# Kernel tuning notes

Measured on AMD Instinct MI355X. Metric: run time of the kernel, lower is better.

Reference implementation:

```python
import jax, jax.numpy as jnp
import numpy as np

# Larq ste_sign: forward sign(x) with sign(0)=+1; backward is identity clipped to |x|<=1 (STE).
@jax.custom_vjp
def ste_sign(x):
    return jnp.where(x >= 0, jnp.ones((), x.dtype), -jnp.ones((), x.dtype))

def _ste_fwd(x):
    return ste_sign(x), x

def _ste_bwd(x, g):
    return (g * (jnp.abs(x) <= 1).astype(g.dtype),)

ste_sign.defvjp(_ste_fwd, _ste_bwd)


def setup_inputs() -> dict:
    key = jax.random.key(0)
    k1, k2 = jax.random.split(key)
    x = jax.random.normal(k1, (16, 112, 112, 256), dtype=jnp.float32)      # NHWC
    kernel = jax.random.normal(k2, (3, 3, 256, 1), dtype=jnp.float32) * 0.1  # (kh, kw, C, mult)
    return {"x": x, "kernel": kernel}


def reference(x, kernel):
    # Quantize input and depthwise kernel, then standard depthwise conv (stride 1, SAME, no bias).
    xq = ste_sign(x)
    kq = ste_sign(kernel)
    kh, kw, C, mult = kernel.shape
    rhs = kq.reshape(kh, kw, 1, C * mult)  # HWIO layout for grouped conv
    out = jax.lax.conv_general_dilated(
        xq, rhs,
        window_strides=(1, 1),
        padding="SAME",
        feature_group_count=C,
        dimension_numbers=("NHWC", "HWIO", "NHWC"),
    )
    return out
```

## Files before the change

kernel.cpp:

```cpp
#include <hip/hip_runtime.h>


constexpr int N = 16, H = 112, W = 112, C = 256;
constexpr int TW = 14;
constexpr int COLS = TW + 2;
constexpr int RW = 4;

typedef float f32x4 __attribute__((ext_vector_type(4)));

__global__ __launch_bounds__(256, 4) void bsign_dw3x3_tstore(
        const float* __restrict__ x, const float* __restrict__ k,
        float* __restrict__ out) {
    __shared__ unsigned sig[COLS * C];

    const int lane = threadIdx.x & 63;
    const int wq   = threadIdx.x >> 6;
    const int c0   = lane << 2;
    const int h0   = blockIdx.y * 16;
    const int w0   = blockIdx.x * TW;
    const int n    = blockIdx.z;

    const size_t rowstride = (size_t)W * C;
    const bool ptop = (h0 > 0);
    const bool pbot = (h0 + 16 < H);

    const int ciB = wq << 2;
    const float* xbase = x + (size_t)(n * H + h0 - 1) * rowstride + c0;
    bool cv[4];
    const float* cp[4];
#pragma unroll
    for (int q = 0; q < 4; ++q) {
        const int xc = w0 - 1 + ciB + q;
        cv[q] = (xc >= 0 && xc < W);
        cp[q] = xbase + (ptrdiff_t)xc * (ptrdiff_t)C;
    }
    unsigned sq[4][4] = {{0,0,0,0},{0,0,0,0},{0,0,0,0},{0,0,0,0}};
#pragma unroll
    for (int p = 0; p < 18; ++p) {
        if (p == 0  && !ptop) continue;
        if (p == 17 && !pbot) continue;
        const size_t ro = (size_t)p * rowstride;
#pragma unroll
        for (int q = 0; q < 4; ++q) {
            if (cv[q]) {
                const uint4 v = *reinterpret_cast<const uint4*>(cp[q] + ro);
                sq[q][0] |= (v.x >> 31) << p;
                sq[q][1] |= (v.y >> 31) << p;
                sq[q][2] |= (v.z >> 31) << p;
                sq[q][3] |= (v.w >> 31) << p;
            }
        }
    }
#pragma unroll
    for (int q = 0; q < 4; ++q) {
        uint4 sv; sv.x = sq[q][0]; sv.y = sq[q][1]; sv.z = sq[q][2]; sv.w = sq[q][3];
        *reinterpret_cast<uint4*>(&sig[(ciB + q) * C + c0]) = sv;
    }

    unsigned k3[3][4] = {{0,0,0,0},{0,0,0,0},{0,0,0,0}};
#pragma unroll
    for (int t = 0; t < 9; ++t) {
        const uint4 kv = *reinterpret_cast<const uint4*>(k + t * C + c0);
        const int kr = t / 3, kj = t % 3;
        k3[kj][0] |= (kv.x >> 31) << kr;
        k3[kj][1] |= (kv.y >> 31) << kr;
        k3[kj][2] |= (kv.z >> 31) << kr;
        k3[kj][3] |= (kv.w >> 31) << kr;
    }
    __syncthreads();

    const int hbase = h0 + (wq << 2);
    float* obase = out + (size_t)(n * H + hbase) * rowstride
                       + (size_t)w0 * C + c0;
    const bool ledge = (w0 == 0), redge = (w0 + TW == W);

#pragma unroll
    for (int r = 0; r < RW; ++r) {
        const int h  = hbase + r;
        const unsigned b = (h == 0) ? 6u : (h == H - 1) ? 3u : 7u;
        const int nr = (h == 0 || h == H - 1) ? 2 : 3;
        const int sh = (wq << 2) + r;
        float* orow = obase + (size_t)r * rowstride;

        int t0m2[4], t0m1[4], t1m1[4], tj0[4], tj1[4], tj2[4];

        auto tcol = [&](int ci) {
            const uint4 v = *reinterpret_cast<const uint4*>(&sig[ci * C + c0]);
            const unsigned d[4] = {v.x >> sh, v.y >> sh, v.z >> sh, v.w >> sh};
#pragma unroll
            for (int ch = 0; ch < 4; ++ch) {
                tj0[ch] = nr - 2 * __popc((d[ch] ^ k3[0][ch]) & b);
                tj1[ch] = nr - 2 * __popc((d[ch] ^ k3[1][ch]) & b);
                tj2[ch] = nr - 2 * __popc((d[ch] ^ k3[2][ch]) & b);
            }
        };

        if (ledge) {
#pragma unroll
            for (int ch = 0; ch < 4; ++ch) t0m2[ch] = 0;
        } else {
            tcol(0);
#pragma unroll
            for (int ch = 0; ch < 4; ++ch) t0m2[ch] = tj0[ch];
        }
        tcol(1);
#pragma unroll
        for (int ch = 0; ch < 4; ++ch) { t0m1[ch] = tj0[ch]; t1m1[ch] = tj1[ch]; }

#pragma unroll
        for (int ci = 2; ci < COLS; ++ci) {
            if (ci == COLS - 1 && redge) {
#pragma unroll
                for (int ch = 0; ch < 4; ++ch) tj2[ch] = 0;
            } else {
                tcol(ci);
            }
            f32x4 ov;
#pragma unroll
            for (int ch = 0; ch < 4; ++ch)
                ov[ch] = (float)(t0m2[ch] + t1m1[ch] + tj2[ch]);
            *reinterpret_cast<f32x4*>(orow + (size_t)(ci - 2) * C) = ov;
#pragma unroll
            for (int ch = 0; ch < 4; ++ch) {
                t0m2[ch] = t0m1[ch]; t0m1[ch] = tj0[ch]; t1m1[ch] = tj1[ch];
            }
        }
    }
}

extern "C" void kernel_launch(void* const* d_in, const int* in_sizes, int n_in,
                              void* d_out, int out_size, void* d_ws, size_t ws_size,
                              hipStream_t stream) {
    const float* x = (const float*)d_in[0];
    const float* k = (const float*)d_in[1];
    float* out = (float*)d_out;

    dim3 grid(W / TW, H / 16, N);
    bsign_dw3x3_tstore<<<grid, 256, 0, stream>>>(x, k, out);
}
```

Baseline: 368.6 us.

## Split into sign-packing pass and bit-based conv kernel using workspace

Replaces the fused tiled kernel with two launches. The first packs input signs into 32-bit words in a workspace buffer. The second computes the depthwise conv from the packed bits, one block per row, reading neighbouring rows from global memory. This removes the halo re-reads of full fp32 input and the shared-memory staging. In exchange it adds an extra launch and a workspace round trip, and the conv kernel does scattered 4-byte loads. A direct unfused kernel is kept as a fallback when no workspace is available.

```diff
diff --git a/kernel.cpp b/kernel.cpp
--- a/kernel.cpp
+++ b/kernel.cpp
@@ -2,60 +2,35 @@
 
 
 constexpr int N = 16, H = 112, W = 112, C = 256;
-constexpr int TW = 14;
-constexpr int COLS = TW + 2;
-constexpr int RW = 4;
+constexpr int NWORDS = N * H * W * (C / 32);
 
 typedef float f32x4 __attribute__((ext_vector_type(4)));
 
-__global__ __launch_bounds__(256, 4) void bsign_dw3x3_tstore(
-        const float* __restrict__ x, const float* __restrict__ k,
+__global__ __launch_bounds__(256, 4) void pack_signs(
+        const float* __restrict__ x, unsigned* __restrict__ sw) {
+    const int t = blockIdx.x * 256 + threadIdx.x;
+    const float* p = x + (size_t)t * 32;
+    unsigned wv = 0;
+#pragma unroll
+    for (int i = 0; i < 8; ++i) {
+        const uint4 v = *reinterpret_cast<const uint4*>(p + i * 4);
+        wv |= ((v.x >> 31) << (4 * i))     | ((v.y >> 31) << (4 * i + 1))
+            | ((v.z >> 31) << (4 * i + 2)) | ((v.w >> 31) << (4 * i + 3));
+    }
+    sw[t] = wv;
+}
+
+__global__ __launch_bounds__(256, 4) void conv_from_bits(
+        const unsigned* __restrict__ sw, const float* __restrict__ k,
         float* __restrict__ out) {
-    __shared__ unsigned sig[COLS * C];
-
+    const int h    = blockIdx.x;
+    const int n    = blockIdx.y;
     const int lane = threadIdx.x & 63;
     const int wq   = threadIdx.x >> 6;
+    const int w0   = wq * 28;
     const int c0   = lane << 2;
-    const int h0   = blockIdx.y * 16;
-    const int w0   = blockIdx.x * TW;
-    const int n    = blockIdx.z;
-
-    const size_t rowstride = (size_t)W * C;
-    const bool ptop = (h0 > 0);
-    const bool pbot = (h0 + 16 < H);
-
-    const int ciB = wq << 2;
-    const float* xbase = x + (size_t)(n * H + h0 - 1) * rowstride + c0;
-    bool cv[4];
-    const float* cp[4];
-#pragma unroll
-    for (int q = 0; q < 4; ++q) {
-        const int xc = w0 - 1 + ciB + q;
-        cv[q] = (xc >= 0 && xc < W);
-        cp[q] = xbase + (ptrdiff_t)xc * (ptrdiff_t)C;
-    }
-    unsigned sq[4][4] = {{0,0,0,0},{0,0,0,0},{0,0,0,0},{0,0,0,0}};
-#pragma unroll
-    for (int p = 0; p < 18; ++p) {
-        if (p == 0  && !ptop) continue;
-        if (p == 17 && !pbot) continue;
-        const size_t ro = (size_t)p * rowstride;
-#pragma unroll
-        for (int q = 0; q < 4; ++q) {
-            if (cv[q]) {
-                const uint4 v = *reinterpret_cast<const uint4*>(cp[q] + ro);
-                sq[q][0] |= (v.x >> 31) << p;
-                sq[q][1] |= (v.y >> 31) << p;
-                sq[q][2] |= (v.z >> 31) << p;
-                sq[q][3] |= (v.w >> 31) << p;
-            }
-        }
-    }
-#pragma unroll
-    for (int q = 0; q < 4; ++q) {
-        uint4 sv; sv.x = sq[q][0]; sv.y = sq[q][1]; sv.z = sq[q][2]; sv.w = sq[q][3];
-        *reinterpret_cast<uint4*>(&sig[(ciB + q) * C + c0]) = sv;
-    }
+    const int wk   = lane >> 3;
+    const int nsh  = (lane & 7) << 2;
 
     unsigned k3[3][4] = {{0,0,0,0},{0,0,0,0},{0,0,0,0}};
 #pragma unroll
@@ -67,65 +42,99 @@
         k3[kj][2] |= (kv.z >> 31) << kr;
         k3[kj][3] |= (kv.w >> 31) << kr;
     }
-    __syncthreads();
 
-    const int hbase = h0 + (wq << 2);
-    float* obase = out + (size_t)(n * H + hbase) * rowstride
-                       + (size_t)w0 * C + c0;
-    const bool ledge = (w0 == 0), redge = (w0 + TW == W);
+    const bool htop = (h > 0), hbot = (h < H - 1);
+    const unsigned bm = !htop ? 6u : !hbot ? 3u : 7u;
+    const int nr = (htop && hbot) ? 3 : 2;
 
+    const unsigned* wrow = sw + ((size_t)(n * H + h) * W) * 8 + wk;
+    constexpr ptrdiff_t RS = (ptrdiff_t)W * 8;
+    float* obase = out + (((size_t)(n * H + h) * W) + w0) * C + c0;
+
+    int t0m2[4], t0m1[4], t1m1[4], a0[4], a1[4], a2[4];
+
+    auto tcol = [&](int cc) {
+        const unsigned wc = wrow[(ptrdiff_t)cc * 8];
+        unsigned wm = 0, wp = 0;
+        if (htop) wm = wrow[(ptrdiff_t)cc * 8 - RS];
+        if (hbot) wp = wrow[(ptrdiff_t)cc * 8 + RS];
 #pragma unroll
-    for (int r = 0; r < RW; ++r) {
-        const int h  = hbase + r;
-        const unsigned b = (h == 0) ? 6u : (h == H - 1) ? 3u : 7u;
-        const int nr = (h == 0 || h == H - 1) ? 2 : 3;
-        const int sh = (wq << 2) + r;
-        float* orow = obase + (size_t)r * rowstride;
+        for (int ch = 0; ch < 4; ++ch) {
+            const unsigned cs = ((wm >> (nsh + ch)) & 1u)
+                              | (((wc >> (nsh + ch)) & 1u) << 1)
+                              | (((wp >> (nsh + ch)) & 1u) << 2);
+            a0[ch] = nr - 2 * __popc((cs ^ k3[0][ch]) & bm);
+            a1[ch] = nr - 2 * __popc((cs ^ k3[1][ch]) & bm);
+            a2[ch] = nr - 2 * __popc((cs ^ k3[2][ch]) & bm);
+        }
+    };
 
-        int t0m2[4], t0m1[4], t1m1[4], tj0[4], tj1[4], tj2[4];
+    const bool ledge = (w0 == 0), redge = (w0 + 28 == W);
 
-        auto tcol = [&](int ci) {
-            const uint4 v = *reinterpret_cast<const uint4*>(&sig[ci * C + c0]);
-            const unsigned d[4] = {v.x >> sh, v.y >> sh, v.z >> sh, v.w >> sh};
+    if (ledge) {
 #pragma unroll
-            for (int ch = 0; ch < 4; ++ch) {
-                tj0[ch] = nr - 2 * __popc((d[ch] ^ k3[0][ch]) & b);
-                tj1[ch] = nr - 2 * __popc((d[ch] ^ k3[1][ch]) & b);
-                tj2[ch] = nr - 2 * __popc((d[ch] ^ k3[2][ch]) & b);
-            }
-        };
+        for (int ch = 0; ch < 4; ++ch) t0m2[ch] = 0;
+    } else {
+        tcol(w0 - 1);
+#pragma unroll
+        for (int ch = 0; ch < 4; ++ch) t0m2[ch] = a0[ch];
+    }
+    tcol(w0);
+#pragma unroll
+    for (int ch = 0; ch < 4; ++ch) { t0m1[ch] = a0[ch]; t1m1[ch] = a1[ch]; }
 
-        if (ledge) {
+#pragma unroll 4
+    for (int cc = w0 + 1; cc <= w0 + 28; ++cc) {
+        if (redge && cc == W) {
 #pragma unroll
-            for (int ch = 0; ch < 4; ++ch) t0m2[ch] = 0;
+            for (int ch = 0; ch < 4; ++ch) a2[ch] = 0;
         } else {
-            tcol(0);
+            tcol(cc);
+        }
+        f32x4 ov;
 #pragma unroll
-            for (int ch = 0; ch < 4; ++ch) t0m2[ch] = tj0[ch];
-        }
-        tcol(1);
+        for (int ch = 0; ch < 4; ++ch)
+            ov[ch] = (float)(t0m2[ch] + t1m1[ch] + a2[ch]);
+        *reinterpret_cast<f32x4*>(obase + (size_t)(cc - 1 - w0) * C) = ov;
 #pragma unroll
-        for (int ch = 0; ch < 4; ++ch) { t0m1[ch] = tj0[ch]; t1m1[ch] = tj1[ch]; }
-
-#pragma unroll
-        for (int ci = 2; ci < COLS; ++ci) {
-            if (ci == COLS - 1 && redge) {
-#pragma unroll
-                for (int ch = 0; ch < 4; ++ch) tj2[ch] = 0;
-            } else {
-                tcol(ci);
-            }
-            f32x4 ov;
-#pragma unroll
-            for (int ch = 0; ch < 4; ++ch)
-                ov[ch] = (float)(t0m2[ch] + t1m1[ch] + tj2[ch]);
-            *reinterpret_cast<f32x4*>(orow + (size_t)(ci - 2) * C) = ov;
-#pragma unroll
-            for (int ch = 0; ch < 4; ++ch) {
-                t0m2[ch] = t0m1[ch]; t0m1[ch] = tj0[ch]; t1m1[ch] = tj1[ch];
-            }
+        for (int ch = 0; ch < 4; ++ch) {
+            t0m2[ch] = t0m1[ch]; t0m1[ch] = a0[ch]; t1m1[ch] = a1[ch];
         }
     }
+}
+
+__global__ __launch_bounds__(256) void bsign_direct(
+        const float* __restrict__ x, const float* __restrict__ k,
+        float* __restrict__ out) {
+    const int idx = blockIdx.x * 256 + threadIdx.x;
+    const int c0  = (idx & 63) << 2;
+    const int pos = idx >> 6;
+    const int w   = pos % W;
+    const int h   = (pos / W) % H;
+    const int n   = pos / (W * H);
+
+    int acc[4] = {0, 0, 0, 0};
+#pragma unroll
+    for (int dr = -1; dr <= 1; ++dr) {
+#pragma unroll
+        for (int dc = -1; dc <= 1; ++dc) {
+            const int hh = h + dr, ww = w + dc;
+            if (hh < 0 || hh >= H || ww < 0 || ww >= W) continue;
+            const uint4 xv = *reinterpret_cast<const uint4*>(
+                x + (((size_t)(n * H + hh) * W) + ww) * C + c0);
+            const uint4 kv = *reinterpret_cast<const uint4*>(
+                k + ((dr + 1) * 3 + (dc + 1)) * C + c0);
+            acc[0] += 1 - 2 * (int)((xv.x ^ kv.x) >> 31);
+            acc[1] += 1 - 2 * (int)((xv.y ^ kv.y) >> 31);
+            acc[2] += 1 - 2 * (int)((xv.z ^ kv.z) >> 31);
+            acc[3] += 1 - 2 * (int)((xv.w ^ kv.w) >> 31);
+        }
+    }
+    f32x4 ov;
+#pragma unroll
+    for (int ch = 0; ch < 4; ++ch) ov[ch] = (float)acc[ch];
+    *reinterpret_cast<f32x4*>(
+        out + (((size_t)(n * H + h) * W) + w) * C + c0) = ov;
 }
 
 extern "C" void kernel_launch(void* const* d_in, const int* in_sizes, int n_in,
@@ -135,6 +144,11 @@
     const float* k = (const float*)d_in[1];
     float* out = (float*)d_out;
 
-    dim3 grid(W / TW, H / 16, N);
-    bsign_dw3x3_tstore<<<grid, 256, 0, stream>>>(x, k, out);
+    if (ws_size >= (size_t)NWORDS * 4 && d_ws != nullptr) {
+        unsigned* sw = (unsigned*)d_ws;
+        pack_signs<<<dim3(NWORDS / 256), 256, 0, stream>>>(x, sw);
+        conv_from_bits<<<dim3(H, N), 256, 0, stream>>>(sw, k, out);
+    } else {
+        bsign_direct<<<dim3(N * H * W * 64 / 256), 256, 0, stream>>>(x, k, out);
+    }
 }
```

Measured after the change: 364.2 us. No clear change (-1.2%).
